# Performance work log

Measured on AMD Instinct MI355X. Metric: run time of the kernel, lower is better.

## Reference

```python
import jax, jax.numpy as jnp
import numpy as np

N = 16384      # n_samples
D = 1024       # embedding_size
C = 16         # number of classes (balanced so every anchor has a positive)
MARGIN = 1.0
EPS = 1e-6


def setup_inputs() -> dict:
    rng = np.random.default_rng(0)
    labels = np.arange(N) % C
    rng.shuffle(labels)
    # positive index: same label, different sample (random within-class rotation)
    pos = np.empty(N, dtype=np.int64)
    for c in range(C):
        idx = np.nonzero(labels == c)[0]
        off = rng.integers(1, len(idx), size=len(idx))
        pos[idx] = idx[(np.arange(len(idx)) + off) % len(idx)]
    # negative index: any sample with a different label (rejection-resample on host)
    neg = rng.integers(0, N, size=N)
    while True:
        bad = labels[neg] == labels
        if not bad.any():
            break
        neg[bad] = rng.integers(0, N, size=int(bad.sum()))
    key = jax.random.key(0)
    embeddings = jax.random.normal(key, (N, D), dtype=jnp.float32)
    return {
        "embeddings": embeddings,
        "labels": jnp.asarray(labels, dtype=jnp.int64),
        "pos_idx": jnp.asarray(pos, dtype=jnp.int64),
        "neg_idx": jnp.asarray(neg, dtype=jnp.int64),
    }


def reference(embeddings, labels, pos_idx, neg_idx):
    # F.normalize(p=2, dim=1, eps=1e-6): x / max(||x||_2, eps)
    norm = jnp.sqrt(jnp.sum(embeddings * embeddings, axis=1, keepdims=True))
    e = embeddings / jnp.maximum(norm, EPS)                      # [N, D]

    def pdist(a, b):
        # F.pairwise_distance adds eps to the difference; module adds another +eps
        return jnp.sqrt(jnp.sum((a - b + EPS) ** 2, axis=1)) + EPS

    d_pos = pdist(e, e[pos_idx])                                 # [N]
    d_neg = pdist(e, e[neg_idx])                                 # [N]
    positive_loss = d_pos ** 2
    negative_loss = jnp.maximum(MARGIN - d_neg, EPS) ** 2
    total = jnp.sum(positive_loss) + jnp.sum(negative_loss)
    return total / (2.0 * N)
```

## Files before the change

kernel.cpp:

```cpp
#include <hip/hip_runtime.h>

#define NROWS 16384
#define DIM   1024
#define F4_PER_ROW 256
#define F4_PER_LANE 4
#define MARGIN_F 1.0f
#define EPS_F 1e-6f

__global__ __launch_bounds__(256) void row_loss_kernel(
    const float* __restrict__ emb,
    const int*   __restrict__ pos_idx,
    const int*   __restrict__ neg_idx,
    float*       __restrict__ losses)
{
    const int tid  = threadIdx.x;
    const int lane = tid & 63;
    const int wid  = tid >> 6;
    const int row  = blockIdx.x * 4 + wid;

    const int p = pos_idx[row];
    const int n = neg_idx[row];

    const float4* xi = (const float4*)(emb + (size_t)row * DIM);
    const float4* xp = (const float4*)(emb + (size_t)p   * DIM);
    const float4* xn = (const float4*)(emb + (size_t)n   * DIM);

    float4 a[F4_PER_LANE], b[F4_PER_LANE], c[F4_PER_LANE];
    #pragma unroll
    for (int j = 0; j < F4_PER_LANE; ++j) {
        a[j] = xi[lane + 64 * j];
        b[j] = xp[lane + 64 * j];
        c[j] = xn[lane + 64 * j];
    }

    float ni = 0.f, np_ = 0.f, nn = 0.f;
    #pragma unroll
    for (int j = 0; j < F4_PER_LANE; ++j) {
        ni  = fmaf(a[j].x, a[j].x, ni);  ni  = fmaf(a[j].y, a[j].y, ni);
        ni  = fmaf(a[j].z, a[j].z, ni);  ni  = fmaf(a[j].w, a[j].w, ni);
        np_ = fmaf(b[j].x, b[j].x, np_); np_ = fmaf(b[j].y, b[j].y, np_);
        np_ = fmaf(b[j].z, b[j].z, np_); np_ = fmaf(b[j].w, b[j].w, np_);
        nn  = fmaf(c[j].x, c[j].x, nn);  nn  = fmaf(c[j].y, c[j].y, nn);
        nn  = fmaf(c[j].z, c[j].z, nn);  nn  = fmaf(c[j].w, c[j].w, nn);
    }
    #pragma unroll
    for (int m = 1; m < 64; m <<= 1) {
        ni  += __shfl_xor(ni,  m, 64);
        np_ += __shfl_xor(np_, m, 64);
        nn  += __shfl_xor(nn,  m, 64);
    }
    const float si = 1.0f / fmaxf(sqrtf(ni),  EPS_F);
    const float sp = 1.0f / fmaxf(sqrtf(np_), EPS_F);
    const float sn = 1.0f / fmaxf(sqrtf(nn),  EPS_F);

    float sum_p = 0.f, sum_n = 0.f;
    #pragma unroll
    for (int j = 0; j < F4_PER_LANE; ++j) {
        float t;
        t = fmaf(a[j].x, si, -b[j].x * sp) + EPS_F; sum_p = fmaf(t, t, sum_p);
        t = fmaf(a[j].y, si, -b[j].y * sp) + EPS_F; sum_p = fmaf(t, t, sum_p);
        t = fmaf(a[j].z, si, -b[j].z * sp) + EPS_F; sum_p = fmaf(t, t, sum_p);
        t = fmaf(a[j].w, si, -b[j].w * sp) + EPS_F; sum_p = fmaf(t, t, sum_p);
        t = fmaf(a[j].x, si, -c[j].x * sn) + EPS_F; sum_n = fmaf(t, t, sum_n);
        t = fmaf(a[j].y, si, -c[j].y * sn) + EPS_F; sum_n = fmaf(t, t, sum_n);
        t = fmaf(a[j].z, si, -c[j].z * sn) + EPS_F; sum_n = fmaf(t, t, sum_n);
        t = fmaf(a[j].w, si, -c[j].w * sn) + EPS_F; sum_n = fmaf(t, t, sum_n);
    }
    #pragma unroll
    for (int m = 1; m < 64; m <<= 1) {
        sum_p += __shfl_xor(sum_p, m, 64);
        sum_n += __shfl_xor(sum_n, m, 64);
    }

    if (lane == 0) {
        float d_pos = sqrtf(sum_p) + EPS_F;
        float d_neg = sqrtf(sum_n) + EPS_F;
        float mq = fmaxf(MARGIN_F - d_neg, EPS_F);
        losses[row] = d_pos * d_pos + mq * mq;
    }
}

__global__ __launch_bounds__(1024) void final_reduce_kernel(
    const float* __restrict__ losses,
    float*       __restrict__ out)
{
    const int tid  = threadIdx.x;
    const int lane = tid & 63;
    const int wid  = tid >> 6;

    const float4* l4 = (const float4*)losses;
    float s = 0.0f;
    #pragma unroll
    for (int j = 0; j < 4; ++j) {
        float4 v = l4[tid + 1024 * j];
        s += v.x + v.y + v.z + v.w;
    }
    #pragma unroll
    for (int m = 1; m < 64; m <<= 1) s += __shfl_xor(s, m, 64);

    __shared__ float sm[16];
    if (lane == 0) sm[wid] = s;
    __syncthreads();
    if (tid == 0) {
        float total = 0.f;
        #pragma unroll
        for (int w = 0; w < 16; ++w) total += sm[w];
        out[0] = total / (2.0f * (float)NROWS);
    }
}

extern "C" void kernel_launch(void* const* d_in, const int* in_sizes, int n_in,
                              void* d_out, int out_size, void* d_ws, size_t ws_size,
                              hipStream_t stream) {
    const float* emb = (const float*)d_in[0];
    const int* pos = (const int*)d_in[2];
    const int* neg = (const int*)d_in[3];

    float* losses = (float*)d_ws;
    float* out    = (float*)d_out;

    row_loss_kernel<<<NROWS / 4, 256, 0, stream>>>(emb, pos, neg, losses);
    final_reduce_kernel<<<1, 1024, 0, stream>>>(losses, out);
}
```

Baseline: 110.8 us.

## Precompute inverse row norms and use dot-product distance expansion

Adds a separate kernel that computes each row's inverse L2 norm once. The loss kernel then computes distances from dot products via 2-2*cos instead of forming the normalized differences. This removes redundant norm computation for gathered rows. In exchange it adds an extra full pass over the embeddings and a kernel launch, and it drops the eps term added inside the difference.

Result: slower. 122.3 us (+10.4%).

```diff
diff --git a/kernel.cpp b/kernel.cpp
--- a/kernel.cpp
+++ b/kernel.cpp
@@ -2,13 +2,38 @@
 
 #define NROWS 16384
 #define DIM   1024
-#define F4_PER_ROW 256
-#define F4_PER_LANE 4
 #define MARGIN_F 1.0f
 #define EPS_F 1e-6f
 
+__global__ __launch_bounds__(256) void inv_norm_kernel(
+    const float* __restrict__ emb,
+    float*       __restrict__ inv_norm)
+{
+    const int tid  = threadIdx.x;
+    const int lane = tid & 63;
+    const int wid  = tid >> 6;
+    const int row  = blockIdx.x * 4 + wid;
+
+    const float4* x = (const float4*)(emb + (size_t)row * DIM);
+    float4 a[4];
+    #pragma unroll
+    for (int j = 0; j < 4; ++j) a[j] = x[lane + 64 * j];
+
+    float s = 0.f;
+    #pragma unroll
+    for (int j = 0; j < 4; ++j) {
+        s = fmaf(a[j].x, a[j].x, s); s = fmaf(a[j].y, a[j].y, s);
+        s = fmaf(a[j].z, a[j].z, s); s = fmaf(a[j].w, a[j].w, s);
+    }
+    #pragma unroll
+    for (int m = 1; m < 64; m <<= 1) s += __shfl_xor(s, m, 64);
+
+    if (lane == 0) inv_norm[row] = 1.0f / fmaxf(sqrtf(s), EPS_F);
+}
+
 __global__ __launch_bounds__(256) void row_loss_kernel(
     const float* __restrict__ emb,
+    const float* __restrict__ inv_norm,
     const int*   __restrict__ pos_idx,
     const int*   __restrict__ neg_idx,
     float*       __restrict__ losses)
@@ -21,58 +46,39 @@
     const int p = pos_idx[row];
     const int n = neg_idx[row];
 
+    const float si = inv_norm[row];
+    const float sp = inv_norm[p];
+    const float sn = inv_norm[n];
+
     const float4* xi = (const float4*)(emb + (size_t)row * DIM);
     const float4* xp = (const float4*)(emb + (size_t)p   * DIM);
     const float4* xn = (const float4*)(emb + (size_t)n   * DIM);
 
-    float4 a[F4_PER_LANE], b[F4_PER_LANE], c[F4_PER_LANE];
+    float4 a[4], b[4], c[4];
     #pragma unroll
-    for (int j = 0; j < F4_PER_LANE; ++j) {
+    for (int j = 0; j < 4; ++j) {
         a[j] = xi[lane + 64 * j];
         b[j] = xp[lane + 64 * j];
         c[j] = xn[lane + 64 * j];
     }
 
-    float ni = 0.f, np_ = 0.f, nn = 0.f;
+    float dab = 0.f, dac = 0.f;
     #pragma unroll
-    for (int j = 0; j < F4_PER_LANE; ++j) {
-        ni  = fmaf(a[j].x, a[j].x, ni);  ni  = fmaf(a[j].y, a[j].y, ni);
-        ni  = fmaf(a[j].z, a[j].z, ni);  ni  = fmaf(a[j].w, a[j].w, ni);
-        np_ = fmaf(b[j].x, b[j].x, np_); np_ = fmaf(b[j].y, b[j].y, np_);
-        np_ = fmaf(b[j].z, b[j].z, np_); np_ = fmaf(b[j].w, b[j].w, np_);
-        nn  = fmaf(c[j].x, c[j].x, nn);  nn  = fmaf(c[j].y, c[j].y, nn);
-        nn  = fmaf(c[j].z, c[j].z, nn);  nn  = fmaf(c[j].w, c[j].w, nn);
+    for (int j = 0; j < 4; ++j) {
+        dab = fmaf(a[j].x, b[j].x, dab); dab = fmaf(a[j].y, b[j].y, dab);
+        dab = fmaf(a[j].z, b[j].z, dab); dab = fmaf(a[j].w, b[j].w, dab);
+        dac = fmaf(a[j].x, c[j].x, dac); dac = fmaf(a[j].y, c[j].y, dac);
+        dac = fmaf(a[j].z, c[j].z, dac); dac = fmaf(a[j].w, c[j].w, dac);
     }
     #pragma unroll
     for (int m = 1; m < 64; m <<= 1) {
-        ni  += __shfl_xor(ni,  m, 64);
-        np_ += __shfl_xor(np_, m, 64);
-        nn  += __shfl_xor(nn,  m, 64);
-    }
-    const float si = 1.0f / fmaxf(sqrtf(ni),  EPS_F);
-    const float sp = 1.0f / fmaxf(sqrtf(np_), EPS_F);
-    const float sn = 1.0f / fmaxf(sqrtf(nn),  EPS_F);
-
-    float sum_p = 0.f, sum_n = 0.f;
-    #pragma unroll
-    for (int j = 0; j < F4_PER_LANE; ++j) {
-        float t;
-        t = fmaf(a[j].x, si, -b[j].x * sp) + EPS_F; sum_p = fmaf(t, t, sum_p);
-        t = fmaf(a[j].y, si, -b[j].y * sp) + EPS_F; sum_p = fmaf(t, t, sum_p);
-        t = fmaf(a[j].z, si, -b[j].z * sp) + EPS_F; sum_p = fmaf(t, t, sum_p);
-        t = fmaf(a[j].w, si, -b[j].w * sp) + EPS_F; sum_p = fmaf(t, t, sum_p);
-        t = fmaf(a[j].x, si, -c[j].x * sn) + EPS_F; sum_n = fmaf(t, t, sum_n);
-        t = fmaf(a[j].y, si, -c[j].y * sn) + EPS_F; sum_n = fmaf(t, t, sum_n);
-        t = fmaf(a[j].z, si, -c[j].z * sn) + EPS_F; sum_n = fmaf(t, t, sum_n);
-        t = fmaf(a[j].w, si, -c[j].w * sn) + EPS_F; sum_n = fmaf(t, t, sum_n);
-    }
-    #pragma unroll
-    for (int m = 1; m < 64; m <<= 1) {
-        sum_p += __shfl_xor(sum_p, m, 64);
-        sum_n += __shfl_xor(sum_n, m, 64);
+        dab += __shfl_xor(dab, m, 64);
+        dac += __shfl_xor(dac, m, 64);
     }
 
     if (lane == 0) {
+        float sum_p = fmaxf(2.0f - 2.0f * si * sp * dab, 0.0f);
+        float sum_n = fmaxf(2.0f - 2.0f * si * sn * dac, 0.0f);
         float d_pos = sqrtf(sum_p) + EPS_F;
         float d_neg = sqrtf(sum_n) + EPS_F;
         float mq = fmaxf(MARGIN_F - d_neg, EPS_F);
@@ -116,9 +122,11 @@
     const int* pos = (const int*)d_in[2];
     const int* neg = (const int*)d_in[3];
 
-    float* losses = (float*)d_ws;
-    float* out    = (float*)d_out;
+    float* inv_norm = (float*)d_ws;
+    float* losses   = (float*)d_ws + NROWS;
+    float* out      = (float*)d_out;
 
-    row_loss_kernel<<<NROWS / 4, 256, 0, stream>>>(emb, pos, neg, losses);
+    inv_norm_kernel<<<NROWS / 4, 256, 0, stream>>>(emb, inv_norm);
+    row_loss_kernel<<<NROWS / 4, 256, 0, stream>>>(emb, inv_norm, pos, neg, losses);
     final_reduce_kernel<<<1, 1024, 0, stream>>>(losses, out);
 }
```
